# Kernel optimization log

Hardware: AMD Instinct MI355X
Metric: run time of the kernel (lower is better)

Reference implementation:

```python
import jax, jax.numpy as jnp
import numpy as np

B, L, N_IN, N_STATE = 32, 4096, 8, 8
C_IN, C_OUT = N_IN + N_STATE, N_STATE
H, M, N_LAYERS = 64, 64, 4


def setup_inputs() -> dict:
    key = jax.random.key(0)
    ks = jax.random.split(key, 16)
    s = 0.02
    return {
        "u": jax.random.normal(ks[0], (B, L, N_IN), jnp.float32),
        "z": jax.random.normal(ks[1], (B, N_STATE), jnp.float32),
        "t": jax.random.uniform(ks[2], (B, 1), jnp.float32),
        "w_lift": jax.random.normal(ks[3], (H, C_IN), jnp.float32) * s,
        "b_lift": jnp.zeros((H,), jnp.float32),
        "spec_wr": jax.random.normal(ks[4], (N_LAYERS, H, H, M), jnp.float32) / (H),
        "spec_wi": jax.random.normal(ks[5], (N_LAYERS, H, H, M), jnp.float32) / (H),
        "w_skip": jax.random.normal(ks[6], (N_LAYERS, H, H), jnp.float32) * s,
        "b_skip": jnp.zeros((N_LAYERS, H), jnp.float32),
        "w_p1": jax.random.normal(ks[7], (2 * H, H), jnp.float32) * s,
        "b_p1": jnp.zeros((2 * H,), jnp.float32),
        "w_p2": jax.random.normal(ks[8], (C_OUT, 2 * H), jnp.float32) * s,
        "b_p2": jnp.zeros((C_OUT,), jnp.float32),
    }


def _fno_forward(u, z, w_lift, b_lift, spec_wr, spec_wi, w_skip, b_skip, w_p1, b_p1, w_p2, b_p2):
    b, l, _ = u.shape
    rep_z = jnp.broadcast_to(z[:, None, :], (b, l, z.shape[1]))
    x = jnp.concatenate([u, rep_z], axis=-1)          # [B, L, C_in]
    x = jnp.transpose(x, (0, 2, 1))                   # [B, C_in, L]
    # lifting (1x1 conv)
    x = jnp.einsum("bcl,hc->bhl", x, w_lift) + b_lift[None, :, None]
    n_layers, _, _, m = spec_wr.shape
    for i in range(n_layers):
        xf = jnp.fft.rfft(x, axis=-1)                 # [B, H, L//2+1] complex
        w = spec_wr[i] + 1j * spec_wi[i]              # [H, H, M]
        of = jnp.einsum("bim,oim->bom", xf[..., :m], w)
        of = jnp.pad(of, ((0, 0), (0, 0), (0, xf.shape[-1] - m)))
        xs = jnp.fft.irfft(of, n=l, axis=-1)          # [B, H, L]
        sk = jnp.einsum("bil,oi->bol", x, w_skip[i]) + b_skip[i][None, :, None]
        x = xs + sk
        if i < n_layers - 1:
            x = jax.nn.gelu(x)
    # projection: H -> 2H -> C_out (1x1 convs)
    x = jax.nn.gelu(jnp.einsum("bhl,ph->bpl", x, w_p1) + b_p1[None, :, None])
    x = jnp.einsum("bpl,op->bol", x, w_p2) + b_p2[None, :, None]
    outs = jnp.transpose(x, (0, 2, 1))                # [B, L, C_out]
    return outs[:, -1, :]                             # [B, C_out]


def reference(u, z, t, w_lift, b_lift, spec_wr, spec_wi, w_skip, b_skip, w_p1, b_p1, w_p2, b_p2):
    # t is accepted by the original forward but unused in FNOProjection
    return _fno_forward(u, z, w_lift, b_lift, spec_wr, spec_wi, w_skip, b_skip, w_p1, b_p1, w_p2, b_p2)
```

## Files before the change

### kernel.cpp

```cpp
#include <hip/hip_runtime.h>
#include <math.h>

typedef _Float16 f16;
typedef f16  f16x2 __attribute__((ext_vector_type(2)));
typedef f16  f16x4 __attribute__((ext_vector_type(4)));
typedef f16  f16x8 __attribute__((ext_vector_type(8)));
typedef float f32x4 __attribute__((ext_vector_type(4)));

#define F4(p)  (*(float4*)(p))
#define CF4(p) (*(const float4*)(p))

namespace {
constexpr int LL = 4096;
constexpr int HH = 64;
constexpr int NCH = 16;

__device__ __forceinline__ float gelu_fast(float x) {
    float inner = 0.7978845608028654f * (x + 0.044715f * x * x * x);
    float e = __expf(-2.0f * inner);
    return x / (1.0f + e);
}

__device__ __forceinline__ f32x4 mfma16(f16x8 a, f16x8 b, f32x4 c) {
    return __builtin_amdgcn_mfma_f32_16x16x32_f16(a, b, c, 0, 0, 0);
}
}

__global__ __launch_bounds__(256) void k_init(const float* __restrict__ u,
                                              const float* __restrict__ z,
                                              const float* __restrict__ wl,
                                              const float* __restrict__ bl,
                                              const float* __restrict__ wsk,
                                              const float* __restrict__ wr,
                                              const float* __restrict__ wi,
                                              f16* __restrict__ Tdt,
                                              f16* __restrict__ Ttr,
                                              f16* __restrict__ wskh,
                                              f16* __restrict__ wrh,
                                              f16* __restrict__ wih,
                                              f16* __restrict__ XT0) {
    const int bid = blockIdx.x;
    const int t = threadIdx.x;
    if (bid < 512) {
        const int b = bid >> 4;
        const int l0 = (bid & 15) * 256;
        constexpr int IP = 260;
        __shared__ float in_s[16 * IP];
        __shared__ float wsh[64 * 16];
        __shared__ float bsh[64];
        for (int i = t; i < 1024; i += 256) wsh[i] = wl[i];
        if (t < 64) bsh[t] = bl[t];
#pragma unroll
        for (int q = 0; q < 2; ++q) {
            int f = t + q * 256;
            int l = f >> 1, cq = (f & 1) * 4;
            float4 v = CF4(u + ((size_t)b * LL + l0 + l) * 8 + cq);
            in_s[(cq + 0) * IP + l] = v.x;
            in_s[(cq + 1) * IP + l] = v.y;
            in_s[(cq + 2) * IP + l] = v.z;
            in_s[(cq + 3) * IP + l] = v.w;
        }
        for (int f = t; f < 8 * 256; f += 256) {
            int c = f >> 8, l = f & 255;
            in_s[(8 + c) * IP + l] = z[b * 8 + c];
        }
        __syncthreads();
        const int hg = t >> 5, lsub = t & 31;
        float acc[8][8] = {};
        for (int c = 0; c < 16; ++c) {
            float wv[8], inv[8];
#pragma unroll
            for (int i = 0; i < 8; ++i) wv[i] = wsh[(hg * 8 + i) * 16 + c];
#pragma unroll
            for (int j = 0; j < 8; ++j) inv[j] = in_s[c * IP + lsub + 32 * j];
#pragma unroll
            for (int i = 0; i < 8; ++i)
#pragma unroll
                for (int j = 0; j < 8; ++j) acc[i][j] += wv[i] * inv[j];
        }
#pragma unroll
        for (int j = 0; j < 8; ++j) {
            __attribute__((aligned(16))) f16 hv[8];
#pragma unroll
            for (int i = 0; i < 8; ++i) hv[i] = (f16)(acc[i][j] + bsh[hg * 8 + i]);
            int l = l0 + lsub + 32 * j;
            F4(XT0 + ((size_t)b * LL + l) * HH + hg * 8) = CF4(hv);
        }
    } else if (bid < 1536) {
        const int tb = bid - 512;
        const float w0 = 6.283185307179586f / 4096.0f;
        {
            int m = tb >> 4;
            int l = ((tb & 15) << 8) + t;
            float s, c;
            sincosf((float)((l * m) & 4095) * w0, &s, &c);
            Tdt[(size_t)(2 * m) * LL + l]     = (f16)c;
            Tdt[(size_t)(2 * m + 1) * LL + l] = (f16)(-s);
        }
        {
            int l = tb * 4 + (t >> 6);
            int m = t & 63;
            float s, c;
            sincosf((float)((l * m) & 4095) * w0, &s, &c);
            const float sc = 1.0f / 4096.0f;
            f16x2 pv;
            pv.x = (f16)((m == 0) ? sc : 2.0f * sc * c);
            pv.y = (f16)((m == 0) ? 0.0f : -2.0f * sc * s);
            *(f16x2*)(Ttr + (size_t)l * 128 + 2 * m) = pv;
        }
        if (tb < 64) {
            int idx = tb * 256 + t;
            wskh[idx] = (f16)wsk[idx];
        }
    } else {
        const int cb = bid - 1536;
        size_t base = (size_t)cb * 1024 + t * 4;
        float4 vr = CF4(wr + base);
        float4 vi = CF4(wi + base);
        f16x4 hr, hi;
        hr.x = (f16)vr.x; hr.y = (f16)vr.y; hr.z = (f16)vr.z; hr.w = (f16)vr.w;
        hi.x = (f16)vi.x; hi.y = (f16)vi.y; hi.z = (f16)vi.z; hi.w = (f16)vi.w;
        *(f16x4*)(wrh + base) = hr;
        *(f16x4*)(wih + base) = hi;
    }
}

__global__ __launch_bounds__(256) void k_dft(const f16* __restrict__ XT,
                                             const f16* __restrict__ Tdt,
                                             f16* __restrict__ Y) {
    __shared__ f16 Asl[32 * 72];
    __shared__ f16 Bsl[128 * 72];
    const int t = threadIdx.x;
    const int ch = blockIdx.x >> 1, h0 = (blockIdx.x & 1) * 32, b = blockIdx.y;
    const int lane = t & 63, wid = t >> 6;
    const int mh = (wid & 1) * 16, n0 = (wid >> 1) * 64;
    const int fm = lane & 15, fq = lane >> 4;
    f32x4 acc[4] = {};
    for (int k0 = 0; k0 < 256; k0 += 64) {
        const int l0 = ch * 256 + k0;
        __syncthreads();
        {
            int seg = t >> 6;
            f16x8 v = *(const f16x8*)(XT + ((size_t)b * LL + l0 + lane) * HH + h0 + seg * 8);
#pragma unroll
            for (int i = 0; i < 8; ++i) Asl[(seg * 8 + i) * 72 + lane] = v[i];
        }
#pragma unroll
        for (int p = 0; p < 4; ++p) {
            int r = (t >> 3) + p * 32;
            F4(&Bsl[r * 72 + (t & 7) * 8]) = CF4(Tdt + (size_t)r * LL + l0 + (t & 7) * 8);
        }
        __syncthreads();
#pragma unroll
        for (int ks = 0; ks < 64; ks += 32) {
            f16x8 a = *(const f16x8*)&Asl[(mh + fm) * 72 + ks + fq * 8];
#pragma unroll
            for (int j = 0; j < 4; ++j) {
                f16x8 bj = *(const f16x8*)&Bsl[(n0 + j * 16 + fm) * 72 + ks + fq * 8];
                acc[j] = mfma16(a, bj, acc[j]);
            }
        }
    }
    f16* yp = Y + ((size_t)ch * 2048 + b * HH + h0) * 128;
#pragma unroll
    for (int j = 0; j < 4; ++j)
#pragma unroll
        for (int r = 0; r < 4; ++r)
            yp[(size_t)(mh + fq * 4 + r) * 128 + n0 + j * 16 + fm] = (f16)acc[j][r];
}

__global__ __launch_bounds__(256) void k_spec(const f16* __restrict__ Y,
                                              const f16* __restrict__ wrh,
                                              const f16* __restrict__ wih,
                                              f16* __restrict__ Ofh, int layer) {
    __shared__ float xsh[64 * 128];
    const int t = threadIdx.x;
    const int b = blockIdx.x;
    const int og = blockIdx.y;
    {
#pragma unroll
        for (int i = 0; i < 4; ++i) {
            int g = t + i * 256;
            float s[8] = {};
#pragma unroll
            for (int c = 0; c < NCH; ++c) {
                f16x8 v = *(const f16x8*)(Y + ((size_t)c * 2048 + b * HH) * 128 + g * 8);
#pragma unroll
                for (int e = 0; e < 8; ++e) s[e] += (float)v[e];
            }
#pragma unroll
            for (int e = 0; e < 8; ++e) xsh[g * 8 + e] = s[e];
        }
    }
    __syncthreads();
    const int m = t & 63, osub = t >> 6;
    const int o = og * 4 + osub;
    const f16* wrp = wrh + ((size_t)layer * HH + o) * HH * 64 + m;
    const f16* wip = wih + ((size_t)layer * HH + o) * HH * 64 + m;
    float are = 0.0f, aim = 0.0f;
    const float2* xs2 = (const float2*)xsh;
#pragma unroll 8
    for (int i = 0; i < 64; ++i) {
        float2 xv = xs2[i * 64 + m];
        float wrv = (float)wrp[(size_t)i * 64];
        float wiv = (float)wip[(size_t)i * 64];
        are += xv.x * wrv - xv.y * wiv;
        aim += xv.x * wiv + xv.y * wrv;
    }
    f16x2 ov; ov.x = (f16)are; ov.y = (f16)aim;
    *(f16x2*)(Ofh + ((size_t)b * HH + o) * 128 + 2 * m) = ov;
}

__global__ __launch_bounds__(512, 4) void k_fused(const f16* __restrict__ Ofh,
                                                  const f16* __restrict__ XTold,
                                                  const f16* __restrict__ Ttr,
                                                  const f16* __restrict__ wskh,
                                                  const float* __restrict__ bsk,
                                                  const f16* __restrict__ Tdt,
                                                  f16* __restrict__ XTn,
                                                  f16* __restrict__ Y,
                                                  int layer) {
    __shared__ f16 XA[64 * 136];
    __shared__ f16 Asl[64 * 200];
    __shared__ f16 Bsl[128 * 72];
    __shared__ float bss[64];
    const int t = threadIdx.x;
    const int lc = blockIdx.x, b = blockIdx.y;
    const int lane = t & 63, wid = t >> 6;
    const int ow = (wid & 1) * 32;
    const int n0 = (wid >> 1) * 32;
    const int fm = lane & 15, fq = lane >> 4;
    {
        int seg = t & 15, row = t >> 4;
#pragma unroll
        for (int p = 0; p < 2; ++p) {
            int r = row + p * 32;
            F4(&Asl[r * 200 + seg * 8]) = CF4(Ofh + ((size_t)(b * HH + r)) * 128 + seg * 8);
        }
        int sg8 = t & 7, r8 = t >> 3;
        F4(&Asl[r8 * 200 + 128 + sg8 * 8]) =
            CF4(wskh + ((size_t)(layer * HH + r8)) * HH + sg8 * 8);
        if (t < 64) bss[t] = bsk[layer * HH + t];
    }
    f32x4 Yac[2][2] = {};
    for (int ls = 0; ls < 2; ++ls) {
        const int l0g = lc * 256 + ls * 128;
        f32x4 acc[2][2] = {};
#pragma unroll
        for (int k0 = 0; k0 < 192; k0 += 64) {
            __syncthreads();
#pragma unroll
            for (int p = 0; p < 2; ++p) {
                int item = t + p * 512;
                int r = item >> 3, sg = item & 7;
                const f16* src = (k0 < 128)
                    ? (Ttr + (size_t)(l0g + r) * 128 + k0 + sg * 8)
                    : (XTold + ((size_t)b * LL + l0g + r) * HH + sg * 8);
                F4(&Bsl[r * 72 + sg * 8]) = CF4(src);
            }
            __syncthreads();
#pragma unroll
            for (int ks = 0; ks < 64; ks += 32) {
                f16x8 a0 = *(const f16x8*)&Asl[(ow + fm) * 200 + k0 + ks + fq * 8];
                f16x8 a1 = *(const f16x8*)&Asl[(ow + 16 + fm) * 200 + k0 + ks + fq * 8];
#pragma unroll
                for (int j = 0; j < 2; ++j) {
                    f16x8 bj = *(const f16x8*)&Bsl[(n0 + j * 16 + fm) * 72 + ks + fq * 8];
                    acc[0][j] = mfma16(a0, bj, acc[0][j]);
                    acc[1][j] = mfma16(a1, bj, acc[1][j]);
                }
            }
        }
        __syncthreads();
#pragma unroll
        for (int i = 0; i < 2; ++i)
#pragma unroll
            for (int r = 0; r < 4; ++r) {
                int row = ow + i * 16 + fq * 4 + r;
                float bias = bss[row];
#pragma unroll
                for (int j = 0; j < 2; ++j) {
                    int lcn = n0 + j * 16 + fm;
                    f16 hv = (f16)gelu_fast(acc[i][j][r] + bias);
                    XA[row * 136 + lcn] = hv;
                    Bsl[lcn * 72 + row] = hv;
                }
            }
        __syncthreads();
        if (layer < 2) {
#pragma unroll
            for (int p = 0; p < 2; ++p) {
                int item = t + p * 512;
                int r = item >> 3, sg = item & 7;
                F4(XTn + ((size_t)b * LL + l0g + r) * HH + sg * 8) = CF4(&Bsl[r * 72 + sg * 8]);
            }
        } else if (lc == NCH - 1 && ls == 1) {
            if (t < 64) XTn[((size_t)b * LL + (LL - 1)) * HH + t] = Bsl[127 * 72 + t];
        }
        __syncthreads();
#pragma unroll
        for (int c = 0; c < 2; ++c) {
            if (c) __syncthreads();
#pragma unroll
            for (int p = 0; p < 2; ++p) {
                int item = t + p * 512;
                int r = item >> 3, sg = item & 7;
                F4(&Bsl[r * 72 + sg * 8]) = CF4(Tdt + (size_t)r * LL + l0g + c * 64 + sg * 8);
            }
            __syncthreads();
#pragma unroll
            for (int ks = 0; ks < 64; ks += 32) {
                f16x8 a0 = *(const f16x8*)&XA[(ow + fm) * 136 + c * 64 + ks + fq * 8];
                f16x8 a1 = *(const f16x8*)&XA[(ow + 16 + fm) * 136 + c * 64 + ks + fq * 8];
#pragma unroll
                for (int j = 0; j < 2; ++j) {
                    f16x8 bj = *(const f16x8*)&Bsl[(n0 + j * 16 + fm) * 72 + ks + fq * 8];
                    Yac[0][j] = mfma16(a0, bj, Yac[0][j]);
                    Yac[1][j] = mfma16(a1, bj, Yac[1][j]);
                }
            }
        }
    }
    f16* yp = Y + ((size_t)lc * 2048 + (size_t)b * HH) * 128;
#pragma unroll
    for (int i = 0; i < 2; ++i)
#pragma unroll
        for (int j = 0; j < 2; ++j)
#pragma unroll
            for (int r = 0; r < 4; ++r)
                yp[(size_t)(ow + i * 16 + fq * 4 + r) * 128 + n0 + j * 16 + fm] =
                    (f16)Yac[i][j][r];
}

__global__ __launch_bounds__(128) void k_final(const f16* __restrict__ Ofh,
                                               const f16* __restrict__ XT3,
                                               const f16* __restrict__ Ttr,
                                               const float* __restrict__ wsk,
                                               const float* __restrict__ bsk,
                                               const float* __restrict__ wp1,
                                               const float* __restrict__ bp1,
                                               const float* __restrict__ wp2,
                                               const float* __restrict__ bp2,
                                               float* __restrict__ out) {
    __shared__ float ofs[64 * 129];
    __shared__ float wsks[64 * 65];
    __shared__ float wp1s[128 * 65];
    __shared__ float tl[128], xl[64], x4[64], y[128];
    const int b = blockIdx.x, t = threadIdx.x;
    {
#pragma unroll
        for (int i = 0; i < 8; ++i) {
            int g = t + i * 128;
            f16x8 v = *(const f16x8*)(Ofh + (size_t)b * HH * 128 + g * 8);
            int o = g >> 4, k0 = (g & 15) * 8;
#pragma unroll
            for (int e = 0; e < 8; ++e) ofs[o * 129 + k0 + e] = (float)v[e];
        }
    }
    {
        const float* src = wsk + 3 * HH * HH;
#pragma unroll
        for (int i = 0; i < 8; ++i) {
            int g = t + i * 128;
            float4 v = CF4(src + g * 4);
            int o = g >> 4, c0 = (g & 15) * 4;
            F4(&wsks[o * 65 + c0]) = v;
        }
    }
    {
#pragma unroll
        for (int i = 0; i < 16; ++i) {
            int g = t + i * 128;
            float4 v = CF4(wp1 + g * 4);
            int p = g >> 4, c0 = (g & 15) * 4;
            F4(&wp1s[p * 65 + c0]) = v;
        }
    }
    tl[t] = (float)Ttr[(size_t)(LL - 1) * 128 + t];
    if (t < 64) xl[t] = (float)XT3[((size_t)b * LL + (LL - 1)) * HH + t];
    __syncthreads();
    if (t < 64) {
        const int o = t;
        float acc = bsk[3 * HH + o];
        for (int k = 0; k < 128; ++k) acc += ofs[o * 129 + k] * tl[k];
        for (int i = 0; i < 64; ++i) acc += wsks[o * 65 + i] * xl[i];
        x4[o] = acc;
    }
    __syncthreads();
    {
        float acc = bp1[t];
        for (int h = 0; h < 64; ++h) acc += wp1s[t * 65 + h] * x4[h];
        y[t] = gelu_fast(acc);
    }
    __syncthreads();
    if (t < 8) {
        float acc = bp2[t];
        for (int p = 0; p < 128; ++p) acc += wp2[t * 128 + p] * y[p];
        out[b * 8 + t] = acc;
    }
}

extern "C" void kernel_launch(void* const* d_in, const int* in_sizes, int n_in,
                              void* d_out, int out_size, void* d_ws, size_t ws_size,
                              hipStream_t stream) {
    (void)in_sizes; (void)n_in; (void)out_size; (void)ws_size;
    const float* u   = (const float*)d_in[0];
    const float* z   = (const float*)d_in[1];
    const float* wl  = (const float*)d_in[3];
    const float* bl  = (const float*)d_in[4];
    const float* swr = (const float*)d_in[5];
    const float* swi = (const float*)d_in[6];
    const float* wsk = (const float*)d_in[7];
    const float* bsk = (const float*)d_in[8];
    const float* wp1 = (const float*)d_in[9];
    const float* bp1 = (const float*)d_in[10];
    const float* wp2 = (const float*)d_in[11];
    const float* bp2 = (const float*)d_in[12];
    float* out = (float*)d_out;

    f16* ws    = (f16*)d_ws;
    f16* XTa   = ws;
    f16* XTb   = XTa + 8388608;
    f16* Tdt   = XTb + 8388608;
    f16* Ttr   = Tdt + 524288;
    f16* Ofh   = Ttr + 524288;
    f16* wskh  = Ofh + 262144;
    f16* wrh   = wskh + 16384;
    f16* wih   = wrh + 1048576;
    f16* Yb    = wih + 1048576;

    k_init<<<2560, 256, 0, stream>>>(u, z, wl, bl, wsk, swr, swi,
                                     Tdt, Ttr, wskh, wrh, wih, XTa);

    k_dft<<<dim3(32, 32), 256, 0, stream>>>(XTa, Tdt, Yb);

    f16* xtc = XTa; f16* xtn = XTb;
    for (int layer = 0; layer < 4; ++layer) {
        k_spec<<<dim3(32, 16), 256, 0, stream>>>(Yb, wrh, wih, Ofh, layer);
        if (layer < 3) {
            k_fused<<<dim3(16, 32), 512, 0, stream>>>(Ofh, xtc, Ttr, wskh, bsk,
                                                      Tdt, xtn, Yb, layer);
            f16* tmp = xtc; xtc = xtn; xtn = tmp;
        } else {
            k_final<<<32, 128, 0, stream>>>(Ofh, xtc, Ttr, wsk, bsk,
                                            wp1, bp1, wp2, bp2, out);
        }
    }
}
```

Before: 202.9 us.

## Register-prefetch next LDS tile to overlap global loads with MFMA

In the DFT kernel and the fused layer kernel, global loads for the next K-tile are issued into registers before the MFMA loop over the current tile, then written to shared memory after a barrier. This software pipelining hides global memory latency behind matrix math across the reconstruction, skip, and forward-DFT phases. It raises register pressure and adds extra barriers per stage, which may reduce occupancy.

```diff
diff --git a/kernel.cpp b/kernel.cpp
--- a/kernel.cpp
+++ b/kernel.cpp
@@ -135,21 +135,29 @@
     const int lane = t & 63, wid = t >> 6;
     const int mh = (wid & 1) * 16, n0 = (wid >> 1) * 64;
     const int fm = lane & 15, fq = lane >> 4;
+    const int seg = t >> 6;
+    const int br = t >> 3, bcol = (t & 7) * 8;
     f32x4 acc[4] = {};
+    f16x8 rA;
+    float4 rb[4];
+    auto ldAB = [&](int k0) {
+        const int l0 = ch * 256 + k0;
+        rA = *(const f16x8*)(XT + ((size_t)b * LL + l0 + lane) * HH + h0 + seg * 8);
+#pragma unroll
+        for (int p = 0; p < 4; ++p)
+            rb[p] = CF4(Tdt + (size_t)(br + p * 32) * LL + l0 + bcol);
+    };
+    auto wrAB = [&]() {
+#pragma unroll
+        for (int i = 0; i < 8; ++i) Asl[(seg * 8 + i) * 72 + lane] = rA[i];
+#pragma unroll
+        for (int p = 0; p < 4; ++p)
+            F4(&Bsl[(br + p * 32) * 72 + bcol]) = rb[p];
+    };
+    ldAB(0);
+    wrAB();
     for (int k0 = 0; k0 < 256; k0 += 64) {
-        const int l0 = ch * 256 + k0;
-        __syncthreads();
-        {
-            int seg = t >> 6;
-            f16x8 v = *(const f16x8*)(XT + ((size_t)b * LL + l0 + lane) * HH + h0 + seg * 8);
-#pragma unroll
-            for (int i = 0; i < 8; ++i) Asl[(seg * 8 + i) * 72 + lane] = v[i];
-        }
-#pragma unroll
-        for (int p = 0; p < 4; ++p) {
-            int r = (t >> 3) + p * 32;
-            F4(&Bsl[r * 72 + (t & 7) * 8]) = CF4(Tdt + (size_t)r * LL + l0 + (t & 7) * 8);
-        }
+        if (k0 < 192) ldAB(k0 + 64);
         __syncthreads();
 #pragma unroll
         for (int ks = 0; ks < 64; ks += 32) {
@@ -160,6 +168,8 @@
                 acc[j] = mfma16(a, bj, acc[j]);
             }
         }
+        __syncthreads();
+        if (k0 < 192) wrAB();
     }
     f16* yp = Y + ((size_t)ch * 2048 + b * HH + h0) * 128;
 #pragma unroll
@@ -230,6 +240,7 @@
     const int ow = (wid & 1) * 32;
     const int n0 = (wid >> 1) * 32;
     const int fm = lane & 15, fq = lane >> 4;
+    const int br = t >> 3, bcol = (t & 7) * 8;
     {
         int seg = t & 15, row = t >> 4;
 #pragma unroll
@@ -237,40 +248,80 @@
             int r = row + p * 32;
             F4(&Asl[r * 200 + seg * 8]) = CF4(Ofh + ((size_t)(b * HH + r)) * 128 + seg * 8);
         }
-        int sg8 = t & 7, r8 = t >> 3;
-        F4(&Asl[r8 * 200 + 128 + sg8 * 8]) =
-            CF4(wskh + ((size_t)(layer * HH + r8)) * HH + sg8 * 8);
+        F4(&Asl[br * 200 + 128 + bcol]) =
+            CF4(wskh + ((size_t)(layer * HH + br)) * HH + bcol);
         if (t < 64) bss[t] = bsk[layer * HH + t];
     }
+    float4 rB0, rB1;
+    auto ldR = [&](int ls, int c) {
+        const int l0g = lc * 256 + ls * 128;
+        if (c < 2) {
+            rB0 = CF4(Ttr + (size_t)(l0g + br) * 128 + c * 64 + bcol);
+            rB1 = CF4(Ttr + (size_t)(l0g + br + 64) * 128 + c * 64 + bcol);
+        } else {
+            rB0 = CF4(XTold + ((size_t)b * LL + l0g + br) * HH + bcol);
+            rB1 = CF4(XTold + ((size_t)b * LL + l0g + br + 64) * HH + bcol);
+        }
+    };
+    auto ldD = [&](int ls, int c) {
+        const int l0 = lc * 256 + ls * 128 + c * 64;
+        rB0 = CF4(Tdt + (size_t)br * LL + l0 + bcol);
+        rB1 = CF4(Tdt + (size_t)(br + 64) * LL + l0 + bcol);
+    };
+    auto wrB = [&]() {
+        F4(&Bsl[br * 72 + bcol]) = rB0;
+        F4(&Bsl[(br + 64) * 72 + bcol]) = rB1;
+    };
+    f32x4 acc[2][2];
     f32x4 Yac[2][2] = {};
+    auto reconMM = [&](int c) {
+#pragma unroll
+        for (int ks = 0; ks < 64; ks += 32) {
+            f16x8 a0 = *(const f16x8*)&Asl[(ow + fm) * 200 + c * 64 + ks + fq * 8];
+            f16x8 a1 = *(const f16x8*)&Asl[(ow + 16 + fm) * 200 + c * 64 + ks + fq * 8];
+#pragma unroll
+            for (int j = 0; j < 2; ++j) {
+                f16x8 bj = *(const f16x8*)&Bsl[(n0 + j * 16 + fm) * 72 + ks + fq * 8];
+                acc[0][j] = mfma16(a0, bj, acc[0][j]);
+                acc[1][j] = mfma16(a1, bj, acc[1][j]);
+            }
+        }
+    };
+    auto dftMM = [&](int c) {
+#pragma unroll
+        for (int ks = 0; ks < 64; ks += 32) {
+            f16x8 a0 = *(const f16x8*)&XA[(ow + fm) * 136 + c * 64 + ks + fq * 8];
+            f16x8 a1 = *(const f16x8*)&XA[(ow + 16 + fm) * 136 + c * 64 + ks + fq * 8];
+#pragma unroll
+            for (int j = 0; j < 2; ++j) {
+                f16x8 bj = *(const f16x8*)&Bsl[(n0 + j * 16 + fm) * 72 + ks + fq * 8];
+                Yac[0][j] = mfma16(a0, bj, Yac[0][j]);
+                Yac[1][j] = mfma16(a1, bj, Yac[1][j]);
+            }
+        }
+    };
+    ldR(0, 0);
+    __syncthreads();
+    wrB();
+    __syncthreads();
     for (int ls = 0; ls < 2; ++ls) {
         const int l0g = lc * 256 + ls * 128;
-        f32x4 acc[2][2] = {};
-#pragma unroll
-        for (int k0 = 0; k0 < 192; k0 += 64) {
-            __syncthreads();
-#pragma unroll
-            for (int p = 0; p < 2; ++p) {
-                int item = t + p * 512;
-                int r = item >> 3, sg = item & 7;
-                const f16* src = (k0 < 128)
-                    ? (Ttr + (size_t)(l0g + r) * 128 + k0 + sg * 8)
-                    : (XTold + ((size_t)b * LL + l0g + r) * HH + sg * 8);
-                F4(&Bsl[r * 72 + sg * 8]) = CF4(src);
-            }
-            __syncthreads();
-#pragma unroll
-            for (int ks = 0; ks < 64; ks += 32) {
-                f16x8 a0 = *(const f16x8*)&Asl[(ow + fm) * 200 + k0 + ks + fq * 8];
-                f16x8 a1 = *(const f16x8*)&Asl[(ow + 16 + fm) * 200 + k0 + ks + fq * 8];
-#pragma unroll
-                for (int j = 0; j < 2; ++j) {
-                    f16x8 bj = *(const f16x8*)&Bsl[(n0 + j * 16 + fm) * 72 + ks + fq * 8];
-                    acc[0][j] = mfma16(a0, bj, acc[0][j]);
-                    acc[1][j] = mfma16(a1, bj, acc[1][j]);
-                }
-            }
-        }
+#pragma unroll
+        for (int i = 0; i < 2; ++i)
+#pragma unroll
+            for (int j = 0; j < 2; ++j) acc[i][j] = (f32x4){0.f, 0.f, 0.f, 0.f};
+        ldR(ls, 1);
+        reconMM(0);
+        __syncthreads();
+        wrB();
+        __syncthreads();
+        ldR(ls, 2);
+        reconMM(1);
+        __syncthreads();
+        wrB();
+        __syncthreads();
+        ldD(ls, 0);
+        reconMM(2);
         __syncthreads();
 #pragma unroll
         for (int i = 0; i < 2; ++i)
@@ -288,37 +339,26 @@
             }
         __syncthreads();
         if (layer < 2) {
-#pragma unroll
-            for (int p = 0; p < 2; ++p) {
-                int item = t + p * 512;
-                int r = item >> 3, sg = item & 7;
-                F4(XTn + ((size_t)b * LL + l0g + r) * HH + sg * 8) = CF4(&Bsl[r * 72 + sg * 8]);
-            }
+            F4(XTn + ((size_t)b * LL + l0g + br) * HH + bcol) = CF4(&Bsl[br * 72 + bcol]);
+            F4(XTn + ((size_t)b * LL + l0g + br + 64) * HH + bcol) =
+                CF4(&Bsl[(br + 64) * 72 + bcol]);
         } else if (lc == NCH - 1 && ls == 1) {
             if (t < 64) XTn[((size_t)b * LL + (LL - 1)) * HH + t] = Bsl[127 * 72 + t];
         }
         __syncthreads();
-#pragma unroll
-        for (int c = 0; c < 2; ++c) {
-            if (c) __syncthreads();
-#pragma unroll
-            for (int p = 0; p < 2; ++p) {
-                int item = t + p * 512;
-                int r = item >> 3, sg = item & 7;
-                F4(&Bsl[r * 72 + sg * 8]) = CF4(Tdt + (size_t)r * LL + l0g + c * 64 + sg * 8);
-            }
+        wrB();
+        __syncthreads();
+        ldD(ls, 1);
+        dftMM(0);
+        __syncthreads();
+        wrB();
+        __syncthreads();
+        if (ls == 0) ldR(1, 0);
+        dftMM(1);
+        if (ls == 0) {
             __syncthreads();
-#pragma unroll
-            for (int ks = 0; ks < 64; ks += 32) {
-                f16x8 a0 = *(const f16x8*)&XA[(ow + fm) * 136 + c * 64 + ks + fq * 8];
-                f16x8 a1 = *(const f16x8*)&XA[(ow + 16 + fm) * 136 + c * 64 + ks + fq * 8];
-#pragma unroll
-                for (int j = 0; j < 2; ++j) {
-                    f16x8 bj = *(const f16x8*)&Bsl[(n0 + j * 16 + fm) * 72 + ks + fq * 8];
-                    Yac[0][j] = mfma16(a0, bj, Yac[0][j]);
-                    Yac[1][j] = mfma16(a1, bj, Yac[1][j]);
-                }
-            }
+            wrB();
+            __syncthreads();
         }
     }
     f16* yp = Y + ((size_t)lc * 2048 + (size_t)b * HH) * 128;
```

Measured after the change: 217.5 us. 7.2% more time.
